# Kernel tuning notes

Hardware: AMD Instinct MI355X
Metric: run time of the kernel (lower is better)

The kernel has to match this reference:

```python
import jax, jax.numpy as jnp
import numpy as np

N = 2097152  # batch of FP32 bit-vectors

# --- logic gates on {0,1} float spikes (faithful to FullAdder/NOT/OR/AND/MUX neurons) ---

def _xor(a, b):
    return a + b - 2.0 * a * b

def _mux(sel, a, b):  # MUXGate(sel, a, b) = a if sel else b
    return sel * a + (1.0 - sel) * b

def _full_adder(a, b, c):  # returns (sum, carry)
    x = _xor(a, b)
    return _xor(x, c), a * b + c * x

def _shift_hi(v, n):  # output[i] = v[i-n], zeros shifted in at the MSB side
    pad = jnp.zeros(v.shape[:-1] + (n,), v.dtype)
    return jnp.concatenate([pad, v[..., :-n]], axis=-1)


def setup_inputs() -> dict:
    key = jax.random.key(0)
    k1, k2 = jax.random.split(key)
    # random 0/1 bit patterns (binary spikes), FP32 bit layout [sign | 8 exp | 23 mant]
    x = jnp.round(jax.random.uniform(k1, (N, 32), dtype=jnp.float32))
    k = jnp.round(jax.random.uniform(k2, (N, 32), dtype=jnp.float32))
    return {"x": x, "k": k}


def reference(x, k):
    batch = x.shape[:-1]
    zeros = jnp.zeros(batch + (1,), x.dtype)
    ones = jnp.ones(batch + (1,), x.dtype)

    s_x, e_x, m_x = x[..., 0:1], x[..., 1:9], x[..., 9:32]
    s_k, e_k, m_k = k[..., 0:1], k[..., 1:9], k[..., 9:32]

    # shift = e_k - 127 via two's complement: e_k + NOT(127) + 1 (little-endian ripple)
    e_k_le = jnp.flip(e_k, -1)
    const_127_le = jnp.concatenate([ones] * 7 + [zeros], axis=-1)
    not_127_le = 1.0 - const_127_le  # NOTGate chain
    shift_bits = []
    borrow = ones
    for i in range(8):
        s, borrow = _full_adder(e_k_le[..., i:i + 1], not_127_le[..., i:i + 1], borrow)
        shift_bits.append(s)
    shift = jnp.concatenate(shift_bits, -1)  # little-endian unbiased exponent

    # barrel shifter on [implicit-1, top 7 mantissa bits] (big-endian), sel = NOT(shift bit)
    val = jnp.concatenate([ones, m_k[..., 0:7]], axis=-1)
    s_bar0 = 1.0 - shift[..., 0:1]
    s_bar1 = 1.0 - shift[..., 1:2]
    s_bar2 = 1.0 - shift[..., 2:3]
    l0 = _mux(s_bar0, _shift_hi(val, 1), val)
    l1 = _mux(s_bar1, _shift_hi(l0, 2), l0)
    l2 = _mux(s_bar2, _shift_hi(l1, 4), l1)
    k_abs_le = jnp.flip(l2, -1)

    # negate |k| (two's complement): NOT(k_abs) + 1
    not_k = 1.0 - k_abs_le
    neg_bits = []
    carry = ones
    for i in range(8):
        s, carry = _full_adder(not_k[..., i:i + 1], zeros, carry)
        neg_bits.append(s)
    neg_k = jnp.concatenate(neg_bits, -1)

    # pick signed k, add to exponent of x (ripple adder, little-endian)
    k_final = _mux(s_k, neg_k, k_abs_le)
    e_x_le = jnp.flip(e_x, -1)
    e_new_bits = []
    carry = zeros
    for i in range(8):
        s, carry = _full_adder(e_x_le[..., i:i + 1], k_final[..., i:i + 1], carry)
        e_new_bits.append(s)
    e_new = jnp.flip(jnp.concatenate(e_new_bits, -1), -1)

    # k == 0 detection: NOT(OR of exp bits) AND NOT(OR of mantissa bits)
    # OR-reduce of binary bits == 1 - prod(1 - bit); NOT gives prod(1 - bit)
    k_e_zero_n = jnp.prod(1.0 - e_k, axis=-1, keepdims=True)
    k_m_zero_n = jnp.prod(1.0 - m_k, axis=-1, keepdims=True)
    k_is_zero = k_e_zero_n * k_m_zero_n  # ANDGate

    result_scaled = jnp.concatenate([s_x, e_new, m_x], axis=-1)
    # final 32-bit MUX: pass x through unchanged when k == 0
    return _mux(k_is_zero, x, result_scaled)
```

## Files before the change

kernel.cpp:

```cpp
#include <hip/hip_runtime.h>


__device__ __forceinline__ unsigned rev8(unsigned v) {
    return __builtin_bitreverse32(v) >> 24;
}

__global__ __launch_bounds__(256) void spike_scale_kernel(
        const float4* __restrict__ x4,
        const float4* __restrict__ k4,
        float4* __restrict__ o4,
        int nvec) {
    int idx = blockIdx.x * 256 + threadIdx.x;
    if (idx >= nvec) return;

    float4 vx = x4[idx];
    float4 vk = k4[idx];

    unsigned g    = (unsigned)(idx & 7);
    unsigned base = g * 4u;

    unsigned nibx = (unsigned)(vx.x != 0.0f)
                  | ((unsigned)(vx.y != 0.0f) << 1)
                  | ((unsigned)(vx.z != 0.0f) << 2)
                  | ((unsigned)(vx.w != 0.0f) << 3);
    unsigned nibk = (unsigned)(vk.x != 0.0f)
                  | ((unsigned)(vk.y != 0.0f) << 1)
                  | ((unsigned)(vk.z != 0.0f) << 2)
                  | ((unsigned)(vk.w != 0.0f) << 3);

    unsigned long long w = ((unsigned long long)nibx << base)
                         | ((unsigned long long)nibk << (32u + base));
    w |= __shfl_xor(w, 1);
    w |= __shfl_xor(w, 2);
    w |= __shfl_xor(w, 4);

    unsigned xw = (unsigned)w;
    unsigned kw = (unsigned)(w >> 32);

    unsigned ek   = rev8((kw >> 1) & 0xFFu);
    unsigned val  = 0x80u | (__builtin_bitreverse32((kw >> 9) & 0x7Fu) >> 25);
    unsigned s    = (ek - 127u) & 7u;
    unsigned kabs = val >> (7u - s);
    unsigned kfin = (kw & 1u) ? ((0u - kabs) & 0xFFu) : kabs;

    unsigned ex   = rev8((xw >> 1) & 0xFFu);
    unsigned enew = (ex + kfin) & 0xFFu;

    unsigned scaled = (xw & 1u) | (rev8(enew) << 1) | (xw & 0xFFFFFE00u);
    unsigned res    = ((kw & ~1u) == 0u) ? xw : scaled;

    float4 out;
    out.x = (float)((res >> (base + 0u)) & 1u);
    out.y = (float)((res >> (base + 1u)) & 1u);
    out.z = (float)((res >> (base + 2u)) & 1u);
    out.w = (float)((res >> (base + 3u)) & 1u);
    o4[idx] = out;
}

extern "C" void kernel_launch(void* const* d_in, const int* in_sizes, int n_in,
                              void* d_out, int out_size, void* d_ws, size_t ws_size,
                              hipStream_t stream) {
    const float4* x4 = (const float4*)d_in[0];
    const float4* k4 = (const float4*)d_in[1];
    float4* o4 = (float4*)d_out;

    int n_elems = in_sizes[0];
    int nvec    = n_elems / 4;
    int blocks  = (nvec + 255) / 256;

    spike_scale_kernel<<<blocks, 256, 0, stream>>>(x4, k4, o4, nvec);
}
```

Measured before the change: 563.5 us.

## Process two rows per thread quad with DPP reduction and nontemporal stores

```diff
diff --git a/kernel.cpp b/kernel.cpp
--- a/kernel.cpp
+++ b/kernel.cpp
@@ -1,60 +1,90 @@
 #include <hip/hip_runtime.h>
 
 
+typedef float fvec4 __attribute__((ext_vector_type(4)));
+
 __device__ __forceinline__ unsigned rev8(unsigned v) {
     return __builtin_bitreverse32(v) >> 24;
+}
+
+__device__ __forceinline__ unsigned nib4(const float4 v) {
+    return (unsigned)(v.x != 0.0f)
+         | ((unsigned)(v.y != 0.0f) << 1)
+         | ((unsigned)(v.z != 0.0f) << 2)
+         | ((unsigned)(v.w != 0.0f) << 3);
+}
+
+__device__ __forceinline__ unsigned quad_or(unsigned w) {
+    w |= (unsigned)__builtin_amdgcn_update_dpp(0, (int)w, 0xB1, 0xF, 0xF, true);
+    w |= (unsigned)__builtin_amdgcn_update_dpp(0, (int)w, 0x4E, 0xF, 0xF, true);
+    return w;
+}
+
+__device__ __forceinline__ unsigned scale_word(unsigned xw, unsigned kw) {
+    unsigned ek   = rev8((kw >> 1) & 0xFFu);
+    unsigned val  = 0x80u | (__builtin_bitreverse32((kw >> 9) & 0x7Fu) >> 25);
+    unsigned s    = (ek - 127u) & 7u;
+    unsigned kabs = val >> (7u - s);
+    unsigned kfin = (kw & 1u) ? ((0u - kabs) & 0xFFu) : kabs;
+    unsigned ex   = rev8((xw >> 1) & 0xFFu);
+    unsigned enew = (ex + kfin) & 0xFFu;
+    unsigned scaled = (xw & 1u) | (rev8(enew) << 1) | (xw & 0xFFFFFE00u);
+    return ((kw & ~1u) == 0u) ? xw : scaled;
+}
+
+__device__ __forceinline__ fvec4 unpack4(unsigned res, unsigned sh) {
+    fvec4 o;
+    o.x = (float)((res >> (sh + 0u)) & 1u);
+    o.y = (float)((res >> (sh + 1u)) & 1u);
+    o.z = (float)((res >> (sh + 2u)) & 1u);
+    o.w = (float)((res >> (sh + 3u)) & 1u);
+    return o;
 }
 
 __global__ __launch_bounds__(256) void spike_scale_kernel(
         const float4* __restrict__ x4,
         const float4* __restrict__ k4,
         float4* __restrict__ o4,
-        int nvec) {
-    int idx = blockIdx.x * 256 + threadIdx.x;
-    if (idx >= nvec) return;
+        int nrows, int half) {
+    int t  = blockIdx.x * 256 + threadIdx.x;
+    int q0 = t >> 2;
+    if (q0 >= half) return;
+    unsigned g  = (unsigned)(t & 3);
+    unsigned sh = g * 4u;
 
-    float4 vx = x4[idx];
-    float4 vk = k4[idx];
+    int  q1   = q0 + half;
+    bool has1 = (q1 < nrows);
+    int  q1c  = has1 ? q1 : q0;
 
-    unsigned g    = (unsigned)(idx & 7);
-    unsigned base = g * 4u;
+    int i00 = q0 * 8 + (int)g;
+    int i01 = i00 + 4;
+    int i10 = q1c * 8 + (int)g;
+    int i11 = i10 + 4;
 
-    unsigned nibx = (unsigned)(vx.x != 0.0f)
-                  | ((unsigned)(vx.y != 0.0f) << 1)
-                  | ((unsigned)(vx.z != 0.0f) << 2)
-                  | ((unsigned)(vx.w != 0.0f) << 3);
-    unsigned nibk = (unsigned)(vk.x != 0.0f)
-                  | ((unsigned)(vk.y != 0.0f) << 1)
-                  | ((unsigned)(vk.z != 0.0f) << 2)
-                  | ((unsigned)(vk.w != 0.0f) << 3);
+    float4 x00 = x4[i00];
+    float4 x01 = x4[i01];
+    float4 k00 = k4[i00];
+    float4 k01 = k4[i01];
+    float4 x10 = x4[i10];
+    float4 x11 = x4[i11];
+    float4 k10 = k4[i10];
+    float4 k11 = k4[i11];
 
-    unsigned long long w = ((unsigned long long)nibx << base)
-                         | ((unsigned long long)nibk << (32u + base));
-    w |= __shfl_xor(w, 1);
-    w |= __shfl_xor(w, 2);
-    w |= __shfl_xor(w, 4);
+    unsigned xw0 = quad_or((nib4(x00) << sh) | (nib4(x01) << (16u + sh)));
+    unsigned kw0 = quad_or((nib4(k00) << sh) | (nib4(k01) << (16u + sh)));
+    unsigned xw1 = quad_or((nib4(x10) << sh) | (nib4(x11) << (16u + sh)));
+    unsigned kw1 = quad_or((nib4(k10) << sh) | (nib4(k11) << (16u + sh)));
 
-    unsigned xw = (unsigned)w;
-    unsigned kw = (unsigned)(w >> 32);
+    unsigned r0 = scale_word(xw0, kw0);
+    unsigned r1 = scale_word(xw1, kw1);
 
-    unsigned ek   = rev8((kw >> 1) & 0xFFu);
-    unsigned val  = 0x80u | (__builtin_bitreverse32((kw >> 9) & 0x7Fu) >> 25);
-    unsigned s    = (ek - 127u) & 7u;
-    unsigned kabs = val >> (7u - s);
-    unsigned kfin = (kw & 1u) ? ((0u - kabs) & 0xFFu) : kabs;
-
-    unsigned ex   = rev8((xw >> 1) & 0xFFu);
-    unsigned enew = (ex + kfin) & 0xFFu;
-
-    unsigned scaled = (xw & 1u) | (rev8(enew) << 1) | (xw & 0xFFFFFE00u);
-    unsigned res    = ((kw & ~1u) == 0u) ? xw : scaled;
-
-    float4 out;
-    out.x = (float)((res >> (base + 0u)) & 1u);
-    out.y = (float)((res >> (base + 1u)) & 1u);
-    out.z = (float)((res >> (base + 2u)) & 1u);
-    out.w = (float)((res >> (base + 3u)) & 1u);
-    o4[idx] = out;
+    fvec4* ov = (fvec4*)o4;
+    __builtin_nontemporal_store(unpack4(r0, sh),       &ov[i00]);
+    __builtin_nontemporal_store(unpack4(r0, 16u + sh), &ov[i01]);
+    if (has1) {
+        __builtin_nontemporal_store(unpack4(r1, sh),       &ov[i10]);
+        __builtin_nontemporal_store(unpack4(r1, 16u + sh), &ov[i11]);
+    }
 }
 
 extern "C" void kernel_launch(void* const* d_in, const int* in_sizes, int n_in,
@@ -64,9 +94,11 @@
     const float4* k4 = (const float4*)d_in[1];
     float4* o4 = (float4*)d_out;
 
-    int n_elems = in_sizes[0];
-    int nvec    = n_elems / 4;
-    int blocks  = (nvec + 255) / 256;
+    int n_elems  = in_sizes[0];
+    int nrows    = n_elems / 32;
+    int half     = (nrows + 1) / 2;
+    int nthreads = half * 4;
+    int blocks   = (nthreads + 255) / 256;
 
-    spike_scale_kernel<<<blocks, 256, 0, stream>>>(x4, k4, o4, nvec);
+    spike_scale_kernel<<<blocks, 256, 0, stream>>>(x4, k4, o4, nrows, half);
 }
```

New measurement: 595.8 us. 5.7% more time.
